# Optimization experiments

Measured on AMD Instinct MI355X. Metric: run time of the kernel, lower is better.

## Reference

```python
import math
import jax, jax.numpy as jnp
import numpy as np

NUM_GROUPS = 32
EPS = 1e-5


def setup_inputs() -> dict:
    key = jax.random.key(0)
    ks = jax.random.split(key, 4)
    b, c, h, w = 8, 512, 64, 64
    x = jax.random.normal(ks[0], (b, c, h, w), dtype=jnp.float32)
    norm_w = jnp.ones((c,), jnp.float32)
    norm_b = jnp.zeros((c,), jnp.float32)
    qkv_w = jax.random.normal(ks[1], (3 * c, c), dtype=jnp.float32) * (1.0 / math.sqrt(c))
    qkv_b = jnp.zeros((3 * c,), jnp.float32)
    out_w = jax.random.normal(ks[2], (c, c), dtype=jnp.float32) * (1.0 / math.sqrt(c))
    out_b = jnp.zeros((c,), jnp.float32)
    return {"x": x, "norm_w": norm_w, "norm_b": norm_b, "qkv_w": qkv_w,
            "qkv_b": qkv_b, "out_w": out_w, "out_b": out_b}


def reference(x, norm_w, norm_b, qkv_w, qkv_b, out_w, out_b):
    b, c, h, w = x.shape
    L = h * w
    # GroupNorm over (c/g, h, w) per group
    xg = x.reshape(b, NUM_GROUPS, -1)
    mu = xg.mean(axis=-1, keepdims=True)
    var = xg.var(axis=-1, keepdims=True)
    xn = ((xg - mu) * jax.lax.rsqrt(var + EPS)).reshape(b, c, L)
    xn = xn * norm_w[:, None] + norm_b[:, None]
    # 1x1 conv == channel matmul -> qkv [b, 3c, L]
    qkv = jnp.einsum('oc,bcl->bol', qkv_w, xn) + qkv_b[:, None]
    q, k, v = jnp.split(qkv, 3, axis=1)  # each [b, c, L]
    scale = 1.0 / math.sqrt(c)
    attn = jax.nn.softmax(jnp.einsum('bcl,bcs->bls', q, k) * scale, axis=-1)
    o = jnp.einsum('bls,bcs->bcl', attn, v)  # [b, c, L]
    o = jnp.einsum('oc,bcl->bol', out_w, o) + out_b[:, None]
    return o.reshape(b, c, h, w) + x
```

## Files before the change

### kernel.cpp

```cpp
#include <hip/hip_runtime.h>
#include <cstdint>

static constexpr int B_ = 8, C_ = 512, L_ = 4096, NG_ = 32;
static constexpr float RSCALE = 0.04419417382415922f;
static constexpr float RSCALE_LOG2E = 0.0637587149159965f;

using f32x4  = __attribute__((ext_vector_type(4))) float;
using bf16x8 = __attribute__((ext_vector_type(8))) short;

__device__ __forceinline__ uint16_t f2bf(float f) {
  union { float f; uint32_t u; } v{f};
  uint32_t r = (v.u + 0x7fffu + ((v.u >> 16) & 1u)) >> 16;
  return (uint16_t)r;
}

__device__ __forceinline__ void gll16(const uint16_t* g, uint16_t* l) {
  __builtin_amdgcn_global_load_lds((const __attribute__((address_space(1))) uint32_t*)g,
                                   (__attribute__((address_space(3))) uint32_t*)l,
                                   16, 0, 0);
}

__device__ __forceinline__ void bar_lgkm() {
  asm volatile("s_waitcnt lgkmcnt(0)" ::: "memory");
  __builtin_amdgcn_s_barrier();
  asm volatile("" ::: "memory");
}
__device__ __forceinline__ void bar_vm_lgkm() {
  asm volatile("s_waitcnt vmcnt(0) lgkmcnt(0)" ::: "memory");
  __builtin_amdgcn_s_barrier();
  asm volatile("" ::: "memory");
}

__global__ __launch_bounds__(256) void k_cvt_bf16(const float* __restrict__ in,
                                                  uint16_t* __restrict__ out, int n) {
  int i = (blockIdx.x * 256 + threadIdx.x) * 4;
  if (i + 3 < n) {
    float4 v = *(const float4*)(in + i);
    union { uint16_t s[4]; uint2 u; } o;
    o.s[0] = f2bf(v.x); o.s[1] = f2bf(v.y); o.s[2] = f2bf(v.z); o.s[3] = f2bf(v.w);
    *(uint2*)(out + i) = o.u;
  }
}

__global__ __launch_bounds__(256) void k_gnstats(const float* __restrict__ x,
                                                 float* __restrict__ mu, float* __restrict__ rs) {
  int bg = blockIdx.x;
  const float* p = x + (size_t)bg * (16 * L_);
  float s = 0.f, s2 = 0.f;
#pragma unroll 8
  for (int i = 0; i < 64; ++i) {
    float4 v = *(const float4*)(p + (threadIdx.x + i * 256) * 4);
    s  += v.x + v.y + v.z + v.w;
    s2 += v.x * v.x + v.y * v.y + v.z * v.z + v.w * v.w;
  }
  for (int o = 32; o; o >>= 1) { s += __shfl_down(s, o); s2 += __shfl_down(s2, o); }
  __shared__ float as_[4], as2_[4];
  int w = threadIdx.x >> 6;
  if ((threadIdx.x & 63) == 0) { as_[w] = s; as2_[w] = s2; }
  __syncthreads();
  if (threadIdx.x == 0) {
    float S = as_[0] + as_[1] + as_[2] + as_[3];
    float S2 = as2_[0] + as2_[1] + as2_[2] + as2_[3];
    float m = S / 65536.0f;
    float var = S2 / 65536.0f - m * m;
    mu[bg] = m; rs[bg] = rsqrtf(var + 1e-5f);
  }
}

__global__ __launch_bounds__(256) void k_normT(const float* __restrict__ x,
                                               const float* __restrict__ nw, const float* __restrict__ nb,
                                               const float* __restrict__ mu, const float* __restrict__ rs,
                                               uint16_t* __restrict__ xnT) {
  __shared__ __align__(16) uint16_t t[64][72];
  int l0 = blockIdx.x * 64, c0 = blockIdx.y * 64, b = blockIdx.z;
#pragma unroll
  for (int i = 0; i < 4; ++i) {
    int idx = threadIdx.x + i * 256;
    int row = idx >> 4, q = idx & 15;
    int c = c0 + row;
    float m_ = mu[b * NG_ + (c >> 4)], r_ = rs[b * NG_ + (c >> 4)];
    float sc = r_ * nw[c], sh = nb[c] - m_ * sc;
    float4 v = *(const float4*)(x + (size_t)(b * C_ + c) * L_ + l0 + q * 4);
    int lb = q * 4;
    t[lb + 0][row] = f2bf(v.x * sc + sh);
    t[lb + 1][row] = f2bf(v.y * sc + sh);
    t[lb + 2][row] = f2bf(v.z * sc + sh);
    t[lb + 3][row] = f2bf(v.w * sc + sh);
  }
  __syncthreads();
#pragma unroll
  for (int i = 0; i < 2; ++i) {
    int idx = threadIdx.x + i * 256;
    int row = idx >> 3, ch = idx & 7;
    uint4 v = *(const uint4*)(&t[row][ch * 8]);
    *(uint4*)(xnT + (size_t)(b * L_ + l0 + row) * C_ + c0 + ch * 8) = v;
  }
}

template <int MODE>
__global__ __launch_bounds__(256, 2) void k_gemm(const uint16_t* __restrict__ Ag, int lda, long long strideA,
                                                 const uint16_t* __restrict__ Bg, int ldb, long long strideB,
                                                 void* __restrict__ Cg, long long strideC,
                                                 const float* __restrict__ bias,
                                                 const float* __restrict__ resid,
                                                 uint16_t* __restrict__ vout) {
  __shared__ __align__(16) uint16_t Asm[128 * 64], Bsm[128 * 64];
  int b = blockIdx.z;
  int m0 = blockIdx.y * 128, n0 = blockIdx.x * 128;
  const uint16_t* A = Ag + (size_t)b * strideA;
  const uint16_t* Bp = Bg + (size_t)b * strideB;
  int lane = threadIdx.x & 63, w = threadIdx.x >> 6;
  int wm = w >> 1, wn = w & 1;
  int l15 = lane & 15, lhi = lane >> 4;
  f32x4 acc[4][4] = {};
  for (int kt = 0; kt < 512; kt += 64) {
#pragma unroll
    for (int i = 0; i < 4; ++i) {
      int idx = threadIdx.x + i * 256;
      int row = idx >> 3, cs = idx & 7, cg = cs ^ (row & 7);
      *(uint4*)(Asm + row * 64 + cs * 8) = *(const uint4*)(A + (size_t)(m0 + row) * lda + kt + cg * 8);
      *(uint4*)(Bsm + row * 64 + cs * 8) = *(const uint4*)(Bp + (size_t)(n0 + row) * ldb + kt + cg * 8);
    }
    __syncthreads();
#pragma unroll
    for (int kk = 0; kk < 2; ++kk) {
      bf16x8 af[4], bfr[4];
      int chunk = kk * 4 + lhi;
#pragma unroll
      for (int m = 0; m < 4; ++m) {
        int row = wm * 64 + m * 16 + l15;
        af[m] = *(const bf16x8*)(Asm + row * 64 + ((chunk ^ (row & 7)) << 3));
      }
#pragma unroll
      for (int n = 0; n < 4; ++n) {
        int row = wn * 64 + n * 16 + l15;
        bfr[n] = *(const bf16x8*)(Bsm + row * 64 + ((chunk ^ (row & 7)) << 3));
      }
#pragma unroll
      for (int m = 0; m < 4; ++m)
#pragma unroll
        for (int n = 0; n < 4; ++n)
          acc[m][n] = __builtin_amdgcn_mfma_f32_16x16x32_bf16(af[m], bfr[n], acc[m][n], 0, 0, 0);
    }
    __syncthreads();
  }
  if (MODE == 0) {
    const bool isV = (n0 >= 1024);
    if (!isV) {
      uint16_t* Cp = (uint16_t*)Cg + (size_t)b * strideC;
#pragma unroll
      for (int n = 0; n < 4; ++n) {
        int col = n0 + wn * 64 + n * 16 + l15;
        float bs = bias[col];
        float scl = (col < 512) ? RSCALE_LOG2E : 1.0f;
#pragma unroll
        for (int m = 0; m < 4; ++m) {
          int rowb = m0 + wm * 64 + m * 16 + lhi * 4;
#pragma unroll
          for (int r = 0; r < 4; ++r)
            Cp[(size_t)(rowb + r) * 1536 + col] = f2bf((acc[m][n][r] + bs) * scl);
        }
      }
    } else {
      uint16_t* Vp = vout + (size_t)b * (C_ * (size_t)L_);
#pragma unroll
      for (int n = 0; n < 4; ++n) {
        int col = n0 + wn * 64 + n * 16 + l15;
        float bs = bias[col];
        uint16_t* vc = Vp + (size_t)(col - 1024) * L_;
#pragma unroll
        for (int m = 0; m < 4; ++m) {
          int rowb = m0 + wm * 64 + m * 16 + lhi * 4;
          union { uint16_t h[4]; uint2 u; } pk;
#pragma unroll
          for (int r = 0; r < 4; ++r) pk.h[r] = f2bf(acc[m][n][r] + bs);
          *(uint2*)(vc + rowb) = pk.u;
        }
      }
    }
  } else {
    float* Cp = (float*)Cg + (size_t)b * strideC;
    const float* Xp = resid + (size_t)b * strideC;
#pragma unroll
    for (int m = 0; m < 4; ++m) {
      int rowb = m0 + wm * 64 + m * 16 + lhi * 4;
#pragma unroll
      for (int n = 0; n < 4; ++n) {
        int col = n0 + wn * 64 + n * 16 + l15;
#pragma unroll
        for (int r = 0; r < 4; ++r) {
          float v = acc[m][n][r] + bias[rowb + r] + Xp[(size_t)(rowb + r) * 4096 + col];
          Cp[(size_t)(rowb + r) * 4096 + col] = v;
        }
      }
    }
  }
}

__global__ __launch_bounds__(512, 1)
void k_attn(const uint16_t* __restrict__ qkvT,
            const uint16_t* __restrict__ vn,
            uint16_t* __restrict__ ot) {
  __shared__ __align__(16) uint16_t kbuf[2][64 * 512];
  __shared__ __align__(16) uint16_t ps[64 * 64];
  __shared__ __align__(16) float lsh[4][64];

  const int tid = threadIdx.x, lane = tid & 63, w = tid >> 6;
  const int l15 = lane & 15, lhi = lane >> 4;
  const int b = blockIdx.x & 7, q0 = (blockIdx.x >> 3) * 64;
  const int sf = w >> 1, lfp = w & 1;
  const int s3 = l15 & 7;

  const uint16_t* kg = qkvT + (size_t)b * L_ * 1536 + 512;
  const uint16_t* vg = vn + (size_t)b * C_ * L_ + (size_t)(w * 64) * L_;

  const int cswz = (lhi ^ s3) << 3;
  const int offK = (sf * 16 + l15) * 512 + cswz;
  const int pch  = ((((sf << 1) | (lhi >> 1)) ^ s3) << 3) + (lhi & 1) * 4;
  const int psw0 = (lfp * 32 + l15) * 64 + pch;
  const int psw1 = psw0 + 16 * 64;
  int pab[4];
#pragma unroll
  for (int m = 0; m < 4; ++m) pab[m] = (m * 16 + l15) * 64 + cswz;

  bf16x8 qr0[16], qr1[16];
  {
    const uint16_t* qp0 = qkvT + (size_t)(b * L_ + q0 + lfp * 32 + l15) * 1536 + lhi * 8;
    const uint16_t* qp1 = qp0 + 16 * 1536;
#pragma unroll
    for (int kc = 0; kc < 16; ++kc) {
      qr0[kc] = *(const bf16x8*)(qp0 + kc * 32);
      qr1[kc] = *(const bf16x8*)(qp1 + kc * 32);
    }
  }

  const int lswz = lane << 3;
#pragma unroll
  for (int i = 0; i < 8; ++i) {
    int row = w * 8 + i;
    gll16(kg + (size_t)row * 1536 + (lswz ^ (i * 8)), &kbuf[0][row * 512]);
  }

  float lrun0 = 0.0f, lrun1 = 0.0f;
  f32x4 acc[4][4] = {};
  bar_vm_lgkm();

  for (int st = 0; st < 64; ++st) {
    const uint16_t* kc0 = kbuf[st & 1];
    uint16_t* knxt = kbuf[(st + 1) & 1];

    f32x4 sfr0 = {}, sfr1 = {};
    const bf16x8* aK0 = (const bf16x8*)(kc0 + offK);
    const bf16x8* aK1 = (const bf16x8*)(kc0 + (offK ^ 32));
#pragma unroll
    for (int kc2 = 0; kc2 < 8; ++kc2) {
      bf16x8 ak0 = aK0[kc2 * 8];
      sfr0 = __builtin_amdgcn_mfma_f32_16x16x32_bf16(ak0, qr0[kc2 * 2], sfr0, 0, 0, 0);
      sfr1 = __builtin_amdgcn_mfma_f32_16x16x32_bf16(ak0, qr1[kc2 * 2], sfr1, 0, 0, 0);
      bf16x8 ak1 = aK1[kc2 * 8];
      sfr0 = __builtin_amdgcn_mfma_f32_16x16x32_bf16(ak1, qr0[kc2 * 2 + 1], sfr0, 0, 0, 0);
      sfr1 = __builtin_amdgcn_mfma_f32_16x16x32_bf16(ak1, qr1[kc2 * 2 + 1], sfr1, 0, 0, 0);
    }

    bf16x8 vb0[4];
    {
      const uint16_t* vrow = vg + st * 64 + lhi * 8;
#pragma unroll
      for (int n = 0; n < 4; ++n) vb0[n] = *(const bf16x8*)(vrow + (size_t)(n * 16 + l15) * L_);
    }

    float p0[4], p1[4], ps0 = 0.f, ps1 = 0.f;
#pragma unroll
    for (int r = 0; r < 4; ++r) {
      p0[r] = exp2f(sfr0[r]); p1[r] = exp2f(sfr1[r]);
      ps0 += p0[r]; ps1 += p1[r];
    }
    ps0 += __shfl_xor(ps0, 16); ps0 += __shfl_xor(ps0, 32);
    ps1 += __shfl_xor(ps1, 16); ps1 += __shfl_xor(ps1, 32);
    lrun0 += ps0; lrun1 += ps1;

    union { uint16_t h[4]; uint2 u; } pk0, pk1;
#pragma unroll
    for (int r = 0; r < 4; ++r) { pk0.h[r] = f2bf(p0[r]); pk1.h[r] = f2bf(p1[r]); }
    *(uint2*)(ps + psw0) = pk0.u;
    *(uint2*)(ps + psw1) = pk1.u;

    if (st < 63) {
      const uint16_t* kst = kg + (size_t)(st + 1) * 98304 + (size_t)(w * 8) * 1536;
#pragma unroll
      for (int i = 0; i < 8; ++i)
        gll16(kst + (size_t)i * 1536 + (lswz ^ (i * 8)), &knxt[(w * 8 + i) * 512]);
    }

    bar_lgkm();

    bf16x8 vb1[4];
    {
      const uint16_t* vrow = vg + st * 64 + 32 + lhi * 8;
#pragma unroll
      for (int n = 0; n < 4; ++n) vb1[n] = *(const bf16x8*)(vrow + (size_t)(n * 16 + l15) * L_);
    }

    {
      bf16x8 pa[4];
#pragma unroll
      for (int m = 0; m < 4; ++m) pa[m] = *(const bf16x8*)(ps + pab[m]);
#pragma unroll
      for (int m = 0; m < 4; ++m)
#pragma unroll
        for (int n = 0; n < 4; ++n)
          acc[m][n] = __builtin_amdgcn_mfma_f32_16x16x32_bf16(pa[m], vb0[n], acc[m][n], 0, 0, 0);
    }
    {
      bf16x8 pa[4];
#pragma unroll
      for (int m = 0; m < 4; ++m) pa[m] = *(const bf16x8*)(ps + (pab[m] ^ 32));
#pragma unroll
      for (int m = 0; m < 4; ++m)
#pragma unroll
        for (int n = 0; n < 4; ++n)
          acc[m][n] = __builtin_amdgcn_mfma_f32_16x16x32_bf16(pa[m], vb1[n], acc[m][n], 0, 0, 0);
    }

    bar_vm_lgkm();
  }

  if (lhi == 0) {
    lsh[sf][lfp * 32 + l15] = lrun0;
    lsh[sf][lfp * 32 + 16 + l15] = lrun1;
  }
  __syncthreads();
#pragma unroll
  for (int m = 0; m < 4; ++m) {
    f32x4 s0v = *(const f32x4*)(&lsh[0][m * 16 + lhi * 4]);
    f32x4 s1v = *(const f32x4*)(&lsh[1][m * 16 + lhi * 4]);
    f32x4 s2v = *(const f32x4*)(&lsh[2][m * 16 + lhi * 4]);
    f32x4 s3v = *(const f32x4*)(&lsh[3][m * 16 + lhi * 4]);
    f32x4 inv;
#pragma unroll
    for (int r = 0; r < 4; ++r) inv[r] = 1.0f / (s0v[r] + s1v[r] + s2v[r] + s3v[r]);
#pragma unroll
    for (int n = 0; n < 4; ++n) {
      int c = w * 64 + n * 16 + l15;
#pragma unroll
      for (int r = 0; r < 4; ++r) {
        int l = q0 + m * 16 + lhi * 4 + r;
        ot[(size_t)(b * L_ + l) * C_ + c] = f2bf(acc[m][n][r] * inv[r]);
      }
    }
  }
}

extern "C" void kernel_launch(void* const* d_in, const int* in_sizes, int n_in,
                              void* d_out, int out_size, void* d_ws, size_t ws_size,
                              hipStream_t stream) {
  const float* x  = (const float*)d_in[0];
  const float* nw = (const float*)d_in[1];
  const float* nb = (const float*)d_in[2];
  const float* qw = (const float*)d_in[3];
  const float* qb = (const float*)d_in[4];
  const float* ow = (const float*)d_in[5];
  const float* ob = (const float*)d_in[6];
  float* out = (float*)d_out;
  char* ws = (char*)d_ws;

  float*    mu   = (float*)(ws + 0);
  float*    rs   = (float*)(ws + 1024);
  uint16_t* wq   = (uint16_t*)(ws + 4096);
  uint16_t* wo   = (uint16_t*)(ws + 4096 + 1572864);
  uint16_t* xnT  = (uint16_t*)(ws + 2101248);
  uint16_t* qkvT = (uint16_t*)(ws + 35655680);
  uint16_t* vn   = (uint16_t*)(ws + 136318976);
  uint16_t* otb  = (uint16_t*)(ws + 169873408);

  k_cvt_bf16<<<dim3((1536 * 512) / 1024), 256, 0, stream>>>(qw, wq, 1536 * 512);
  k_cvt_bf16<<<dim3((512 * 512) / 1024), 256, 0, stream>>>(ow, wo, 512 * 512);
  k_gnstats<<<dim3(256), 256, 0, stream>>>(x, mu, rs);
  k_normT<<<dim3(64, 8, 8), 256, 0, stream>>>(x, nw, nb, mu, rs, xnT);
  k_gemm<0><<<dim3(12, 32, 8), 256, 0, stream>>>(xnT, 512, (long long)4096 * 512,
                                                 wq, 512, 0LL,
                                                 qkvT, (long long)4096 * 1536, qb, nullptr, vn);
  k_attn<<<dim3(512), 512, 0, stream>>>(qkvT, vn, otb);
  k_gemm<1><<<dim3(32, 4, 8), 256, 0, stream>>>(wo, 512, 0LL,
                                                otb, 512, (long long)4096 * 512,
                                                out, (long long)512 * 4096, ob, x, nullptr);
}
```

Measured before the change: 660.0 us.

## Halve attention block to four waves, each computing twice the work

The attention kernel drops from 8 to 4 waves per block. Each wave now computes a 32-key by 32-query score tile and accumulates a 64x128 output slice, so acc grows to 4x8 fragments. Each wave also loads twice as many K rows and V columns. This gives more reuse per wave and fewer waves contending at barriers, but roughly doubles register pressure (accumulators, Q fragments and V fragments) and leaves fewer waves to hide latency.

```diff
diff --git a/kernel.cpp b/kernel.cpp
--- a/kernel.cpp
+++ b/kernel.cpp
@@ -197,35 +197,41 @@
   }
 }
 
-__global__ __launch_bounds__(512, 1)
+__global__ __launch_bounds__(256, 1)
 void k_attn(const uint16_t* __restrict__ qkvT,
             const uint16_t* __restrict__ vn,
             uint16_t* __restrict__ ot) {
   __shared__ __align__(16) uint16_t kbuf[2][64 * 512];
   __shared__ __align__(16) uint16_t ps[64 * 64];
-  __shared__ __align__(16) float lsh[4][64];
+  __shared__ __align__(16) float lsh[2][64];
 
   const int tid = threadIdx.x, lane = tid & 63, w = tid >> 6;
   const int l15 = lane & 15, lhi = lane >> 4;
   const int b = blockIdx.x & 7, q0 = (blockIdx.x >> 3) * 64;
-  const int sf = w >> 1, lfp = w & 1;
+  const int wl = w & 1;
+  const int wsf = w >> 1;
   const int s3 = l15 & 7;
 
   const uint16_t* kg = qkvT + (size_t)b * L_ * 1536 + 512;
-  const uint16_t* vg = vn + (size_t)b * C_ * L_ + (size_t)(w * 64) * L_;
-
-  const int cswz = (lhi ^ s3) << 3;
-  const int offK = (sf * 16 + l15) * 512 + cswz;
-  const int pch  = ((((sf << 1) | (lhi >> 1)) ^ s3) << 3) + (lhi & 1) * 4;
-  const int psw0 = (lfp * 32 + l15) * 64 + pch;
-  const int psw1 = psw0 + 16 * 64;
+  const uint16_t* vg = vn + (size_t)b * C_ * L_ + (size_t)(w * 128) * L_;
+
+  const int cswz  = (lhi ^ s3) << 3;
+  const int offK0 = (wsf * 32 + l15) * 512 + cswz;
+  const int offK1 = offK0 + 16 * 512;
+  int pswr[2][2];
+#pragma unroll
+  for (int sf = 0; sf < 2; ++sf)
+#pragma unroll
+    for (int lf = 0; lf < 2; ++lf)
+      pswr[sf][lf] = (wl * 32 + lf * 16 + l15) * 64 +
+                     (((wsf * 4 + sf * 2 + (lhi >> 1)) ^ s3) << 3) + (lhi & 1) * 4;
   int pab[4];
 #pragma unroll
   for (int m = 0; m < 4; ++m) pab[m] = (m * 16 + l15) * 64 + cswz;
 
   bf16x8 qr0[16], qr1[16];
   {
-    const uint16_t* qp0 = qkvT + (size_t)(b * L_ + q0 + lfp * 32 + l15) * 1536 + lhi * 8;
+    const uint16_t* qp0 = qkvT + (size_t)(b * L_ + q0 + wl * 32 + l15) * 1536 + lhi * 8;
     const uint16_t* qp1 = qp0 + 16 * 1536;
 #pragma unroll
     for (int kc = 0; kc < 16; ++kc) {
@@ -236,112 +242,115 @@
 
   const int lswz = lane << 3;
 #pragma unroll
-  for (int i = 0; i < 8; ++i) {
-    int row = w * 8 + i;
-    gll16(kg + (size_t)row * 1536 + (lswz ^ (i * 8)), &kbuf[0][row * 512]);
+  for (int i = 0; i < 16; ++i) {
+    int row = w * 16 + i;
+    gll16(kg + (size_t)row * 1536 + (lswz ^ ((i & 7) * 8)), &kbuf[0][row * 512]);
   }
 
   float lrun0 = 0.0f, lrun1 = 0.0f;
-  f32x4 acc[4][4] = {};
+  f32x4 acc[4][8] = {};
   bar_vm_lgkm();
 
   for (int st = 0; st < 64; ++st) {
     const uint16_t* kc0 = kbuf[st & 1];
     uint16_t* knxt = kbuf[(st + 1) & 1];
 
-    f32x4 sfr0 = {}, sfr1 = {};
-    const bf16x8* aK0 = (const bf16x8*)(kc0 + offK);
-    const bf16x8* aK1 = (const bf16x8*)(kc0 + (offK ^ 32));
+    f32x4 s00 = {}, s01 = {}, s10 = {}, s11 = {};
+    const bf16x8* a00 = (const bf16x8*)(kc0 + offK0);
+    const bf16x8* a01 = (const bf16x8*)(kc0 + (offK0 ^ 32));
+    const bf16x8* a10 = (const bf16x8*)(kc0 + offK1);
+    const bf16x8* a11 = (const bf16x8*)(kc0 + (offK1 ^ 32));
 #pragma unroll
     for (int kc2 = 0; kc2 < 8; ++kc2) {
-      bf16x8 ak0 = aK0[kc2 * 8];
-      sfr0 = __builtin_amdgcn_mfma_f32_16x16x32_bf16(ak0, qr0[kc2 * 2], sfr0, 0, 0, 0);
-      sfr1 = __builtin_amdgcn_mfma_f32_16x16x32_bf16(ak0, qr1[kc2 * 2], sfr1, 0, 0, 0);
-      bf16x8 ak1 = aK1[kc2 * 8];
-      sfr0 = __builtin_amdgcn_mfma_f32_16x16x32_bf16(ak1, qr0[kc2 * 2 + 1], sfr0, 0, 0, 0);
-      sfr1 = __builtin_amdgcn_mfma_f32_16x16x32_bf16(ak1, qr1[kc2 * 2 + 1], sfr1, 0, 0, 0);
-    }
-
-    bf16x8 vb0[4];
+      bf16x8 k0 = a00[kc2 * 8];
+      s00 = __builtin_amdgcn_mfma_f32_16x16x32_bf16(k0, qr0[kc2 * 2], s00, 0, 0, 0);
+      s01 = __builtin_amdgcn_mfma_f32_16x16x32_bf16(k0, qr1[kc2 * 2], s01, 0, 0, 0);
+      bf16x8 k1 = a10[kc2 * 8];
+      s10 = __builtin_amdgcn_mfma_f32_16x16x32_bf16(k1, qr0[kc2 * 2], s10, 0, 0, 0);
+      s11 = __builtin_amdgcn_mfma_f32_16x16x32_bf16(k1, qr1[kc2 * 2], s11, 0, 0, 0);
+      bf16x8 k0b = a01[kc2 * 8];
+      s00 = __builtin_amdgcn_mfma_f32_16x16x32_bf16(k0b, qr0[kc2 * 2 + 1], s00, 0, 0, 0);
+      s01 = __builtin_amdgcn_mfma_f32_16x16x32_bf16(k0b, qr1[kc2 * 2 + 1], s01, 0, 0, 0);
+      bf16x8 k1b = a11[kc2 * 8];
+      s10 = __builtin_amdgcn_mfma_f32_16x16x32_bf16(k1b, qr0[kc2 * 2 + 1], s10, 0, 0, 0);
+      s11 = __builtin_amdgcn_mfma_f32_16x16x32_bf16(k1b, qr1[kc2 * 2 + 1], s11, 0, 0, 0);
+    }
+
+    bf16x8 vb[2][8];
     {
       const uint16_t* vrow = vg + st * 64 + lhi * 8;
 #pragma unroll
-      for (int n = 0; n < 4; ++n) vb0[n] = *(const bf16x8*)(vrow + (size_t)(n * 16 + l15) * L_);
-    }
-
-    float p0[4], p1[4], ps0 = 0.f, ps1 = 0.f;
+      for (int n = 0; n < 8; ++n) {
+        vb[0][n] = *(const bf16x8*)(vrow + (size_t)(n * 16 + l15) * L_);
+        vb[1][n] = *(const bf16x8*)(vrow + (size_t)(n * 16 + l15) * L_ + 32);
+      }
+    }
+
+    float p00[4], p01[4], p10[4], p11[4];
+    float ps0 = 0.f, ps1 = 0.f;
 #pragma unroll
     for (int r = 0; r < 4; ++r) {
-      p0[r] = exp2f(sfr0[r]); p1[r] = exp2f(sfr1[r]);
-      ps0 += p0[r]; ps1 += p1[r];
+      p00[r] = exp2f(s00[r]); p10[r] = exp2f(s10[r]);
+      p01[r] = exp2f(s01[r]); p11[r] = exp2f(s11[r]);
+      ps0 += p00[r] + p10[r];
+      ps1 += p01[r] + p11[r];
     }
     ps0 += __shfl_xor(ps0, 16); ps0 += __shfl_xor(ps0, 32);
     ps1 += __shfl_xor(ps1, 16); ps1 += __shfl_xor(ps1, 32);
     lrun0 += ps0; lrun1 += ps1;
 
-    union { uint16_t h[4]; uint2 u; } pk0, pk1;
-#pragma unroll
-    for (int r = 0; r < 4; ++r) { pk0.h[r] = f2bf(p0[r]); pk1.h[r] = f2bf(p1[r]); }
-    *(uint2*)(ps + psw0) = pk0.u;
-    *(uint2*)(ps + psw1) = pk1.u;
+    {
+      union { uint16_t h[4]; uint2 u; } k00, k01, k10, k11;
+#pragma unroll
+      for (int r = 0; r < 4; ++r) {
+        k00.h[r] = f2bf(p00[r]); k01.h[r] = f2bf(p01[r]);
+        k10.h[r] = f2bf(p10[r]); k11.h[r] = f2bf(p11[r]);
+      }
+      *(uint2*)(ps + pswr[0][0]) = k00.u;
+      *(uint2*)(ps + pswr[0][1]) = k01.u;
+      *(uint2*)(ps + pswr[1][0]) = k10.u;
+      *(uint2*)(ps + pswr[1][1]) = k11.u;
+    }
 
     if (st < 63) {
-      const uint16_t* kst = kg + (size_t)(st + 1) * 98304 + (size_t)(w * 8) * 1536;
-#pragma unroll
-      for (int i = 0; i < 8; ++i)
-        gll16(kst + (size_t)i * 1536 + (lswz ^ (i * 8)), &knxt[(w * 8 + i) * 512]);
+      const uint16_t* kst = kg + (size_t)(st + 1) * 98304 + (size_t)(w * 16) * 1536;
+#pragma unroll
+      for (int i = 0; i < 16; ++i)
+        gll16(kst + (size_t)i * 1536 + (lswz ^ ((i & 7) * 8)), &knxt[(w * 16 + i) * 512]);
     }
 
     bar_lgkm();
 
-    bf16x8 vb1[4];
-    {
-      const uint16_t* vrow = vg + st * 64 + 32 + lhi * 8;
-#pragma unroll
-      for (int n = 0; n < 4; ++n) vb1[n] = *(const bf16x8*)(vrow + (size_t)(n * 16 + l15) * L_);
-    }
-
-    {
+#pragma unroll
+    for (int kk = 0; kk < 2; ++kk) {
       bf16x8 pa[4];
 #pragma unroll
-      for (int m = 0; m < 4; ++m) pa[m] = *(const bf16x8*)(ps + pab[m]);
+      for (int m = 0; m < 4; ++m) pa[m] = *(const bf16x8*)(ps + (pab[m] ^ (kk * 32)));
 #pragma unroll
       for (int m = 0; m < 4; ++m)
 #pragma unroll
-        for (int n = 0; n < 4; ++n)
-          acc[m][n] = __builtin_amdgcn_mfma_f32_16x16x32_bf16(pa[m], vb0[n], acc[m][n], 0, 0, 0);
-    }
-    {
-      bf16x8 pa[4];
-#pragma unroll
-      for (int m = 0; m < 4; ++m) pa[m] = *(const bf16x8*)(ps + (pab[m] ^ 32));
-#pragma unroll
-      for (int m = 0; m < 4; ++m)
-#pragma unroll
-        for (int n = 0; n < 4; ++n)
-          acc[m][n] = __builtin_amdgcn_mfma_f32_16x16x32_bf16(pa[m], vb1[n], acc[m][n], 0, 0, 0);
+        for (int n = 0; n < 8; ++n)
+          acc[m][n] = __builtin_amdgcn_mfma_f32_16x16x32_bf16(pa[m], vb[kk][n], acc[m][n], 0, 0, 0);
     }
 
     bar_vm_lgkm();
   }
 
   if (lhi == 0) {
-    lsh[sf][lfp * 32 + l15] = lrun0;
-    lsh[sf][lfp * 32 + 16 + l15] = lrun1;
+    lsh[wsf][wl * 32 + l15] = lrun0;
+    lsh[wsf][wl * 32 + 16 + l15] = lrun1;
   }
   __syncthreads();
 #pragma unroll
   for (int m = 0; m < 4; ++m) {
     f32x4 s0v = *(const f32x4*)(&lsh[0][m * 16 + lhi * 4]);
     f32x4 s1v = *(const f32x4*)(&lsh[1][m * 16 + lhi * 4]);
-    f32x4 s2v = *(const f32x4*)(&lsh[2][m * 16 + lhi * 4]);
-    f32x4 s3v = *(const f32x4*)(&lsh[3][m * 16 + lhi * 4]);
     f32x4 inv;
 #pragma unroll
-    for (int r = 0; r < 4; ++r) inv[r] = 1.0f / (s0v[r] + s1v[r] + s2v[r] + s3v[r]);
-#pragma unroll
-    for (int n = 0; n < 4; ++n) {
-      int c = w * 64 + n * 16 + l15;
+    for (int r = 0; r < 4; ++r) inv[r] = 1.0f / (s0v[r] + s1v[r]);
+#pragma unroll
+    for (int n = 0; n < 8; ++n) {
+      int c = w * 128 + n * 16 + l15;
 #pragma unroll
       for (int r = 0; r < 4; ++r) {
         int l = q0 + m * 16 + lhi * 4 + r;
@@ -380,7 +389,7 @@
   k_gemm<0><<<dim3(12, 32, 8), 256, 0, stream>>>(xnT, 512, (long long)4096 * 512,
                                                  wq, 512, 0LL,
                                                  qkvT, (long long)4096 * 1536, qb, nullptr, vn);
-  k_attn<<<dim3(512), 512, 0, stream>>>(qkvT, vn, otb);
+  k_attn<<<dim3(512), 256, 0, stream>>>(qkvT, vn, otb);
   k_gemm<1><<<dim3(32, 4, 8), 256, 0, stream>>>(wo, 512, 0LL,
                                                 otb, 512, (long long)4096 * 512,
                                                 out, (long long)512 * 4096, ob, x, nullptr);
```

Measured after the change: 685.1 us. 1.04x slower.
